# Optimization experiments

Hardware: AMD Instinct MI355X
Metric: run time of the kernel (lower is better)

## Reference

```python
import jax, jax.numpy as jnp
import numpy as np

N = 12288
IN_CH = 64
OUT_CH = 32


def setup_inputs() -> dict:
    key = jax.random.key(0)
    k_x, k_adj, k_w = jax.random.split(key, 3)
    x = jax.random.normal(k_x, (N, IN_CH), dtype=jnp.float32)
    # binary adjacency matrix (dense form of the sparse edge_index tensor)
    edge_index = jax.random.randint(k_adj, (N, N), 0, 2).astype(jnp.float32)
    # xavier_uniform for weight [in, out]
    limit = float(np.sqrt(6.0 / (IN_CH + OUT_CH)))
    weight = jax.random.uniform(k_w, (IN_CH, OUT_CH), dtype=jnp.float32,
                                minval=-limit, maxval=limit)
    bias = jnp.zeros((OUT_CH,), dtype=jnp.float32)
    return {"x": x, "edge_index": edge_index, "weight": weight, "bias": bias}


def reference(x, edge_index, weight, bias):
    # bgnn_a_norm: add self loops, then per-row norm = 1 / (rowsum^2 - sum(row^2))
    adj = edge_index + jnp.eye(edge_index.shape[0], dtype=edge_index.dtype)
    adj_sq = jnp.square(adj)
    row_sum = adj.sum(axis=-1)            # [N]
    denom = jnp.square(row_sum) - adj_sq.sum(axis=-1)  # [N]
    norm = 1.0 / denom
    norm = jnp.where(jnp.isinf(norm), 0.0, norm)       # [N]

    # bgnn_pool: (adj @ xw)^2 - adj^2 @ xw^2
    xw = x @ weight                        # [N, out]
    s = adj @ xw                           # [N, out]
    out = jnp.square(s) - adj_sq @ jnp.square(xw)

    # norm is a diagonal matrix in the original -> row-wise scale
    out = norm[:, None] * out + bias
    return out
```

## Files before the change

### kernel.cpp

```cpp
#include <hip/hip_runtime.h>


#define NN 12288
#define IN_CH 64
#define OUT_CH 32
#define KC 8
#define KPC (NN / KC)
#define NSTEP (KPC / 32)
#define MB 128
#define NMB (NN / MB)
#define NKSTEP (NN / 32)

typedef __attribute__((ext_vector_type(8))) short short8;
typedef __attribute__((ext_vector_type(4))) float f32x4;

static __device__ __forceinline__ unsigned short f2bf_rn(float f) {
    unsigned int u = __float_as_uint(f);
    u += 0x7fffu + ((u >> 16) & 1u);
    return (unsigned short)(u >> 16);
}

__global__ __launch_bounds__(256) void build_xw(const float* __restrict__ x,
                                                const float* __restrict__ w,
                                                float* __restrict__ XW) {
    int t = blockIdx.x * blockDim.x + threadIdx.x;
    int i = t >> 5;
    int c = t & 31;
    if (i >= NN) return;
    float acc = 0.f;
#pragma unroll
    for (int k4 = 0; k4 < IN_CH / 4; ++k4) {
        f32x4 xv = *(const f32x4*)&x[(size_t)i * IN_CH + k4 * 4];
        acc = fmaf(xv.x, w[(k4 * 4 + 0) * OUT_CH + c], acc);
        acc = fmaf(xv.y, w[(k4 * 4 + 1) * OUT_CH + c], acc);
        acc = fmaf(xv.z, w[(k4 * 4 + 2) * OUT_CH + c], acc);
        acc = fmaf(xv.w, w[(k4 * 4 + 3) * OUT_CH + c], acc);
    }
    XW[(size_t)i * OUT_CH + c] = acc;
}

__global__ __launch_bounds__(256) void packb(const float* __restrict__ XW,
                                             unsigned int* __restrict__ Bp) {
    int idx = blockIdx.x * 256 + threadIdx.x;
    int s = idx >> 9;
    int rem = idx & 511;
    int t = rem >> 6;
    int l = rem & 63;
    int kbase = s * 32 + ((l >> 4) * 8);
    int col = t * 16 + (l & 15);
    int cc = col & 31;
    bool sq = (col & 63) >= 32;
    bool lo = col >= 64;
    unsigned int out[4];
#pragma unroll
    for (int d = 0; d < 4; ++d) {
        unsigned short h[2];
#pragma unroll
        for (int j = 0; j < 2; ++j) {
            float v = XW[(size_t)(kbase + 2 * d + j) * OUT_CH + cc];
            if (sq) v *= v;
            unsigned short hb = f2bf_rn(v);
            if (lo) {
                float hf = __uint_as_float((unsigned int)hb << 16);
                hb = f2bf_rn(v - hf);
            }
            h[j] = hb;
        }
        out[d] = (unsigned int)h[0] | ((unsigned int)h[1] << 16);
    }
    *(uint4*)&Bp[(size_t)idx * 4] = *(uint4*)out;
}

__global__ __launch_bounds__(256) void spmm(const float* __restrict__ E,
                                            const unsigned int* __restrict__ Bp,
                                            float* __restrict__ Ssl,
                                            float* __restrict__ RSsl) {
    const int mb = blockIdx.x % NMB;
    const int kc = blockIdx.x / NMB;
    const int tid = threadIdx.x;
    const int wid = tid >> 6;
    const int lane = tid & 63;
    const int r0 = mb * MB + wid * 32;
    const int row0 = r0 + (lane & 15);
    const int kq = (lane >> 4) * 8;

    f32x4 acc[2][8] = {};
    float rs[2] = {0.f, 0.f};

    const float* e0p = E + (size_t)row0 * NN + kc * KPC + kq;
    const float* e1p = e0p + (size_t)16 * NN;

    for (int s = 0; s < NSTEP; ++s) {
        const int koff = s * 32;
        f32x4 a0 = __builtin_nontemporal_load((const f32x4*)(e0p + koff));
        f32x4 a1 = __builtin_nontemporal_load((const f32x4*)(e0p + koff) + 1);
        f32x4 c0 = __builtin_nontemporal_load((const f32x4*)(e1p + koff));
        f32x4 c1 = __builtin_nontemporal_load((const f32x4*)(e1p + koff) + 1);

        const unsigned int* bp = Bp + (size_t)(kc * NSTEP + s) * 2048 + lane * 4;
        uint4 b[8];
#pragma unroll
        for (int t = 0; t < 8; ++t)
            b[t] = *(const uint4*)(bp + t * 256);

        union { unsigned int u[4]; short8 v; } pa, pb;
        pa.u[0] = (__float_as_uint(a0.x) >> 16) | (__float_as_uint(a0.y) & 0xffff0000u);
        pa.u[1] = (__float_as_uint(a0.z) >> 16) | (__float_as_uint(a0.w) & 0xffff0000u);
        pa.u[2] = (__float_as_uint(a1.x) >> 16) | (__float_as_uint(a1.y) & 0xffff0000u);
        pa.u[3] = (__float_as_uint(a1.z) >> 16) | (__float_as_uint(a1.w) & 0xffff0000u);
        pb.u[0] = (__float_as_uint(c0.x) >> 16) | (__float_as_uint(c0.y) & 0xffff0000u);
        pb.u[1] = (__float_as_uint(c0.z) >> 16) | (__float_as_uint(c0.w) & 0xffff0000u);
        pb.u[2] = (__float_as_uint(c1.x) >> 16) | (__float_as_uint(c1.y) & 0xffff0000u);
        pb.u[3] = (__float_as_uint(c1.z) >> 16) | (__float_as_uint(c1.w) & 0xffff0000u);

        rs[0] += ((a0.x + a0.y) + (a0.z + a0.w)) + ((a1.x + a1.y) + (a1.z + a1.w));
        rs[1] += ((c0.x + c0.y) + (c0.z + c0.w)) + ((c1.x + c1.y) + (c1.z + c1.w));

#pragma unroll
        for (int t = 0; t < 8; ++t) {
            union { uint4 q; short8 v; } bu;
            bu.q = b[t];
            acc[0][t] = __builtin_amdgcn_mfma_f32_16x16x32_bf16(pa.v, bu.v, acc[0][t], 0, 0, 0);
            acc[1][t] = __builtin_amdgcn_mfma_f32_16x16x32_bf16(pb.v, bu.v, acc[1][t], 0, 0, 0);
        }
    }

#pragma unroll
    for (int m = 0; m < 2; ++m) {
        float v = rs[m];
        v += __shfl_xor(v, 16, 64);
        v += __shfl_xor(v, 32, 64);
        if ((lane >> 4) == 0)
            RSsl[(size_t)kc * NN + r0 + m * 16 + (lane & 15)] = v;
    }

    const size_t sbase = (((size_t)kc * NMB + mb) * 4 + wid) * 2;
#pragma unroll
    for (int m = 0; m < 2; ++m) {
#pragma unroll
        for (int t = 0; t < 4; ++t) {
            f32x4 v = acc[m][t] + acc[m][t + 4];
            *(f32x4*)&Ssl[((sbase + m) * 4 + t) * 256 + lane * 4] = v;
        }
    }
}

__global__ __launch_bounds__(256) void epi(const float* __restrict__ E,
                                           const float* __restrict__ XW,
                                           const float* __restrict__ Ssl,
                                           const float* __restrict__ RSsl,
                                           const float* __restrict__ bias,
                                           float* __restrict__ out) {
    int tt0 = blockIdx.x * blockDim.x + threadIdx.x;
    int i = tt0 >> 5;
    int c = tt0 & 31;
    if (i >= NN) return;
    const int mb = i >> 7;
    const int wid = (i >> 5) & 3;
    const int m = (i >> 4) & 1;
    const int lane_s = ((i >> 2) & 3) * 16 + (c & 15);
    const int r = i & 3;
    const int ts = c >> 4;
    float s = 0.f, tsum = 0.f, rse = 0.f;
#pragma unroll
    for (int kc = 0; kc < KC; ++kc) {
        const size_t base = ((((size_t)kc * NMB + mb) * 4 + wid) * 2 + m) * 4;
        s    += Ssl[(base + ts) * 256 + lane_s * 4 + r];
        tsum += Ssl[(base + 2 + ts) * 256 + lane_s * 4 + r];
        rse  += RSsl[(size_t)kc * NN + i];
    }
    const float eii = E[(size_t)i * NN + i];
    const float xwc = XW[(size_t)i * OUT_CH + c];
    const float xw2c = xwc * xwc;
    s += xwc;
    tsum += (eii != 0.f ? 3.f : 1.f) * xw2c;
    const float rsa = rse + 1.f;
    const float d1 = eii + 1.f;
    const float sumsq = rse - eii + d1 * d1;
    const float denom = rsa * rsa - sumsq;
    const float nrm = (denom == 0.f) ? 0.f : 1.f / denom;
    out[(size_t)i * OUT_CH + c] = nrm * (s * s - tsum) + bias[c];
}

extern "C" void kernel_launch(void* const* d_in, const int* in_sizes, int n_in,
                              void* d_out, int out_size, void* d_ws, size_t ws_size,
                              hipStream_t stream) {
    const float* x    = (const float*)d_in[0];
    const float* E    = (const float*)d_in[1];
    const float* w    = (const float*)d_in[2];
    const float* bias = (const float*)d_in[3];
    float* out = (float*)d_out;

    float* XW = (float*)d_ws;
    unsigned int* Bp = (unsigned int*)(XW + (size_t)NN * OUT_CH);
    float* Ssl = (float*)(Bp + (size_t)NKSTEP * 512 * 4);
    float* RSsl = Ssl + (size_t)KC * NMB * 4 * 2 * 4 * 256;

    build_xw<<<NN * OUT_CH / 256, 256, 0, stream>>>(x, w, XW);
    packb<<<NKSTEP * 512 / 256, 256, 0, stream>>>(XW, Bp);
    spmm<<<NMB * KC, 256, 0, stream>>>(E, Bp, Ssl, RSsl);
    epi<<<NN * OUT_CH / 256, 256, 0, stream>>>(E, XW, Ssl, RSsl, bias, out);
}
```

Baseline: 836.3 us.

## Split spmm row tiles across eight waves and software-prefetch adjacency loads

The spmm kernel now runs 512 threads per block, and each wave handles 16 rows instead of 32. That halves accumulator registers per wave and raises the wave count available to hide memory latency on the 600MB adjacency stream. It also adds a register double-buffer that prefetches the next step's adjacency values, and it swaps nontemporal loads for ordinary ones. The Ssl partial-sum layout and the epilogue indexing change to match. The cost is that each wave now reloads the same B fragments for fewer rows, doubling B-operand traffic per adjacency byte, and dropping the nontemporal hint may pollute the cache.

```diff
diff --git a/kernel.cpp b/kernel.cpp
--- a/kernel.cpp
+++ b/kernel.cpp
@@ -71,77 +71,65 @@
     *(uint4*)&Bp[(size_t)idx * 4] = *(uint4*)out;
 }
 
-__global__ __launch_bounds__(256) void spmm(const float* __restrict__ E,
-                                            const unsigned int* __restrict__ Bp,
-                                            float* __restrict__ Ssl,
-                                            float* __restrict__ RSsl) {
+__global__ __launch_bounds__(512, 4) void spmm(const float* __restrict__ E,
+                                               const unsigned int* __restrict__ Bp,
+                                               float* __restrict__ Ssl,
+                                               float* __restrict__ RSsl) {
     const int mb = blockIdx.x % NMB;
     const int kc = blockIdx.x / NMB;
     const int tid = threadIdx.x;
-    const int wid = tid >> 6;
+    const int w = tid >> 6;
     const int lane = tid & 63;
-    const int r0 = mb * MB + wid * 32;
+    const int r0 = mb * MB + w * 16;
     const int row0 = r0 + (lane & 15);
     const int kq = (lane >> 4) * 8;
 
-    f32x4 acc[2][8] = {};
-    float rs[2] = {0.f, 0.f};
+    f32x4 acc[8] = {};
+    float rs = 0.f;
 
-    const float* e0p = E + (size_t)row0 * NN + kc * KPC + kq;
-    const float* e1p = e0p + (size_t)16 * NN;
+    const float* ep = E + (size_t)row0 * NN + kc * KPC + kq;
+
+    f32x4 a0n = *(const f32x4*)(ep);
+    f32x4 a1n = *(const f32x4*)(ep + 4);
 
     for (int s = 0; s < NSTEP; ++s) {
-        const int koff = s * 32;
-        f32x4 a0 = __builtin_nontemporal_load((const f32x4*)(e0p + koff));
-        f32x4 a1 = __builtin_nontemporal_load((const f32x4*)(e0p + koff) + 1);
-        f32x4 c0 = __builtin_nontemporal_load((const f32x4*)(e1p + koff));
-        f32x4 c1 = __builtin_nontemporal_load((const f32x4*)(e1p + koff) + 1);
-
+        f32x4 a0 = a0n, a1 = a1n;
+        if (s + 1 < NSTEP) {
+            a0n = *(const f32x4*)(ep + (s + 1) * 32);
+            a1n = *(const f32x4*)(ep + (s + 1) * 32 + 4);
+        }
         const unsigned int* bp = Bp + (size_t)(kc * NSTEP + s) * 2048 + lane * 4;
         uint4 b[8];
 #pragma unroll
         for (int t = 0; t < 8; ++t)
             b[t] = *(const uint4*)(bp + t * 256);
 
-        union { unsigned int u[4]; short8 v; } pa, pb;
+        union { unsigned int u[4]; short8 v; } pa;
         pa.u[0] = (__float_as_uint(a0.x) >> 16) | (__float_as_uint(a0.y) & 0xffff0000u);
         pa.u[1] = (__float_as_uint(a0.z) >> 16) | (__float_as_uint(a0.w) & 0xffff0000u);
         pa.u[2] = (__float_as_uint(a1.x) >> 16) | (__float_as_uint(a1.y) & 0xffff0000u);
         pa.u[3] = (__float_as_uint(a1.z) >> 16) | (__float_as_uint(a1.w) & 0xffff0000u);
-        pb.u[0] = (__float_as_uint(c0.x) >> 16) | (__float_as_uint(c0.y) & 0xffff0000u);
-        pb.u[1] = (__float_as_uint(c0.z) >> 16) | (__float_as_uint(c0.w) & 0xffff0000u);
-        pb.u[2] = (__float_as_uint(c1.x) >> 16) | (__float_as_uint(c1.y) & 0xffff0000u);
-        pb.u[3] = (__float_as_uint(c1.z) >> 16) | (__float_as_uint(c1.w) & 0xffff0000u);
 
-        rs[0] += ((a0.x + a0.y) + (a0.z + a0.w)) + ((a1.x + a1.y) + (a1.z + a1.w));
-        rs[1] += ((c0.x + c0.y) + (c0.z + c0.w)) + ((c1.x + c1.y) + (c1.z + c1.w));
+        rs += ((a0.x + a0.y) + (a0.z + a0.w)) + ((a1.x + a1.y) + (a1.z + a1.w));
 
 #pragma unroll
         for (int t = 0; t < 8; ++t) {
             union { uint4 q; short8 v; } bu;
             bu.q = b[t];
-            acc[0][t] = __builtin_amdgcn_mfma_f32_16x16x32_bf16(pa.v, bu.v, acc[0][t], 0, 0, 0);
-            acc[1][t] = __builtin_amdgcn_mfma_f32_16x16x32_bf16(pb.v, bu.v, acc[1][t], 0, 0, 0);
+            acc[t] = __builtin_amdgcn_mfma_f32_16x16x32_bf16(pa.v, bu.v, acc[t], 0, 0, 0);
         }
     }
 
+    rs += __shfl_xor(rs, 16, 64);
+    rs += __shfl_xor(rs, 32, 64);
+    if (lane < 16)
+        RSsl[(size_t)kc * NN + r0 + lane] = rs;
+
+    const size_t base = (((size_t)kc * NMB + mb) * 8 + w) * 4;
 #pragma unroll
-    for (int m = 0; m < 2; ++m) {
-        float v = rs[m];
-        v += __shfl_xor(v, 16, 64);
-        v += __shfl_xor(v, 32, 64);
-        if ((lane >> 4) == 0)
-            RSsl[(size_t)kc * NN + r0 + m * 16 + (lane & 15)] = v;
-    }
-
-    const size_t sbase = (((size_t)kc * NMB + mb) * 4 + wid) * 2;
-#pragma unroll
-    for (int m = 0; m < 2; ++m) {
-#pragma unroll
-        for (int t = 0; t < 4; ++t) {
-            f32x4 v = acc[m][t] + acc[m][t + 4];
-            *(f32x4*)&Ssl[((sbase + m) * 4 + t) * 256 + lane * 4] = v;
-        }
+    for (int t = 0; t < 4; ++t) {
+        f32x4 v = acc[t] + acc[t + 4];
+        *(f32x4*)&Ssl[(base + t) * 256 + lane * 4] = v;
     }
 }
 
@@ -156,15 +144,15 @@
     int c = tt0 & 31;
     if (i >= NN) return;
     const int mb = i >> 7;
-    const int wid = (i >> 5) & 3;
-    const int m = (i >> 4) & 1;
-    const int lane_s = ((i >> 2) & 3) * 16 + (c & 15);
-    const int r = i & 3;
+    const int w = (i >> 4) & 7;
+    const int rw = i & 15;
+    const int lane_s = (rw >> 2) * 16 + (c & 15);
+    const int r = rw & 3;
     const int ts = c >> 4;
     float s = 0.f, tsum = 0.f, rse = 0.f;
 #pragma unroll
     for (int kc = 0; kc < KC; ++kc) {
-        const size_t base = ((((size_t)kc * NMB + mb) * 4 + wid) * 2 + m) * 4;
+        const size_t base = (((size_t)kc * NMB + mb) * 8 + w) * 4;
         s    += Ssl[(base + ts) * 256 + lane_s * 4 + r];
         tsum += Ssl[(base + 2 + ts) * 256 + lane_s * 4 + r];
         rse  += RSsl[(size_t)kc * NN + i];
@@ -194,10 +182,10 @@
     float* XW = (float*)d_ws;
     unsigned int* Bp = (unsigned int*)(XW + (size_t)NN * OUT_CH);
     float* Ssl = (float*)(Bp + (size_t)NKSTEP * 512 * 4);
-    float* RSsl = Ssl + (size_t)KC * NMB * 4 * 2 * 4 * 256;
+    float* RSsl = Ssl + (size_t)KC * NMB * 8 * 4 * 256;
 
     build_xw<<<NN * OUT_CH / 256, 256, 0, stream>>>(x, w, XW);
     packb<<<NKSTEP * 512 / 256, 256, 0, stream>>>(XW, Bp);
-    spmm<<<NMB * KC, 256, 0, stream>>>(E, Bp, Ssl, RSsl);
+    spmm<<<NMB * KC, 512, 0, stream>>>(E, Bp, Ssl, RSsl);
     epi<<<NN * OUT_CH / 256, 256, 0, stream>>>(E, XW, Ssl, RSsl, bias, out);
 }
```

After: 880.3 us. +5.3%, slower.
